# Optimization experiments

Hardware: AMD Instinct MI355X
Metric: run time of the kernel (lower is better)

## Reference

```python
import jax, jax.numpy as jnp
import numpy as np

GN_GROUPS = 32
GN_EPS = 1e-5


def conv3x3(x, w, b=None):
    # x: [B,C,H,W], w: [O,I,3,3]
    y = jax.lax.conv_general_dilated(x, w, (1, 1), 'SAME',
                                     dimension_numbers=('NCHW', 'OIHW', 'NCHW'))
    if b is not None:
        y = y + b[None, :, None, None]
    return y


def group_norm(x, gamma, beta):
    B, C, H, W = x.shape
    xg = x.reshape(B, GN_GROUPS, C // GN_GROUPS, H, W)
    mu = xg.mean(axis=(2, 3, 4), keepdims=True)
    var = ((xg - mu) ** 2).mean(axis=(2, 3, 4), keepdims=True)
    xn = ((xg - mu) * jax.lax.rsqrt(var + GN_EPS)).reshape(B, C, H, W)
    return xn * gamma[None, :, None, None] + beta[None, :, None, None]


def tower(x, ws, gammas, betas):
    # ws: [n_conv, C, C, 3, 3]; conv(bias=False) -> GroupNorm -> ReLU, n_conv times
    for i in range(ws.shape[0]):
        x = jax.nn.relu(group_norm(conv3x3(x, ws[i]), gammas[i], betas[i]))
    return x


def setup_inputs() -> dict:
    key = jax.random.key(0)
    ks = jax.random.split(key, 20)
    C, n_conv, n_fg = 256, 4, 20  # n_class - 1 = 20
    prior = 0.01
    B = 2
    sizes = [(100, 100), (50, 50), (25, 25), (13, 13), (7, 7)]
    inp = {}
    for i, (h, w) in enumerate(sizes):
        inp[f'feat{i}'] = jax.random.normal(ks[i], (B, C, h, w), dtype=jnp.float32)
    std = 0.01  # init_conv_std
    inp['cls_tw_w'] = std * jax.random.normal(ks[5], (n_conv, C, C, 3, 3), dtype=jnp.float32)
    inp['cls_tw_g'] = jnp.ones((n_conv, C), dtype=jnp.float32)
    inp['cls_tw_b'] = jnp.zeros((n_conv, C), dtype=jnp.float32)
    inp['box_tw_w'] = std * jax.random.normal(ks[6], (n_conv, C, C, 3, 3), dtype=jnp.float32)
    inp['box_tw_g'] = jnp.ones((n_conv, C), dtype=jnp.float32)
    inp['box_tw_b'] = jnp.zeros((n_conv, C), dtype=jnp.float32)
    inp['cls_pred_w'] = std * jax.random.normal(ks[7], (n_fg, C, 3, 3), dtype=jnp.float32)
    prior_bias = -np.log((1.0 - prior) / prior)
    inp['cls_pred_b'] = jnp.full((n_fg,), prior_bias, dtype=jnp.float32)
    inp['box_pred_w'] = std * jax.random.normal(ks[8], (4, C, 3, 3), dtype=jnp.float32)
    inp['box_pred_b'] = jnp.zeros((4,), dtype=jnp.float32)
    inp['ctr_pred_w'] = std * jax.random.normal(ks[9], (1, C, 3, 3), dtype=jnp.float32)
    inp['ctr_pred_b'] = jnp.zeros((1,), dtype=jnp.float32)
    inp['scales'] = jnp.ones((5,), dtype=jnp.float32)
    return inp


def reference(feat0, feat1, feat2, feat3, feat4,
              cls_tw_w, cls_tw_g, cls_tw_b,
              box_tw_w, box_tw_g, box_tw_b,
              cls_pred_w, cls_pred_b,
              box_pred_w, box_pred_b,
              ctr_pred_w, ctr_pred_b,
              scales):
    feats = [feat0, feat1, feat2, feat3, feat4]
    logits, bboxes, centers = [], [], []
    for i, feat in enumerate(feats):
        c = tower(feat, cls_tw_w, cls_tw_g, cls_tw_b)
        logits.append(conv3x3(c, cls_pred_w, cls_pred_b))
        centers.append(conv3x3(c, ctr_pred_w, ctr_pred_b))
        b = tower(feat, box_tw_w, box_tw_g, box_tw_b)
        bboxes.append(jnp.exp(conv3x3(b, box_pred_w, box_pred_b) * scales[i]))
    return tuple(logits + bboxes + centers)
```

## Files before the change

### kernel.cpp

```cpp
#include <hip/hip_runtime.h>
#include <hip/hip_bf16.h>
#include <cstdint>

typedef unsigned short u16;
typedef __attribute__((ext_vector_type(8))) short short8;
typedef __attribute__((ext_vector_type(4))) float floatx4;

#define PA_TOTAL 13696
#define CCH 256
#define KTOT 2304

struct Tables {
  int H[5], W[5], P[5], base[5], tile0[5];
  int lb[5], bb[5], cb[5];
};
struct FeatPtrs { const float* f[5]; };
struct ConvArgs {
  const u16* X[2];
  const u16* Wt[2];
  const u16* zbuf;
  u16* outB[2];
  float* stats;
  float* dout;
  const float* biasCls; const float* biasCtr; const float* biasBox; const float* scales;
};

__device__ __forceinline__ u16 f2bf(float f) {
  union { float f; unsigned u; } v; v.f = f;
  unsigned r = v.u + 0x7fffu + ((v.u >> 16) & 1u);
  return (u16)(r >> 16);
}
__device__ __forceinline__ float bf2f(u16 h) {
  union { unsigned u; float f; } v; v.u = ((unsigned)h) << 16;
  return v.f;
}

__device__ __forceinline__ void gl2lds16(const u16* g, u16* l) {
  __builtin_amdgcn_global_load_lds((const __attribute__((address_space(1))) unsigned int*)g,
                                   (__attribute__((address_space(3))) unsigned int*)l, 16, 0, 0);
}

__global__ void reorder_rows(const float* __restrict__ src, u16* __restrict__ out) {
  __shared__ float row[KTOT];
  const int r = blockIdx.x;
  const float* s = src + (size_t)r * KTOT;
  u16* o = out + (size_t)r * KTOT;
#pragma unroll
  for (int j = 0; j < 9; ++j) row[threadIdx.x + j * 256] = s[threadIdx.x + j * 256];
  __syncthreads();
#pragma unroll
  for (int j = 0; j < 9; ++j) {
    int k = threadIdx.x + j * 256;
    o[k] = f2bf(row[(k & 255) * 9 + (k >> 8)]);
  }
}

__global__ void reorder_pred_cls(const float* __restrict__ cls_w, const float* __restrict__ ctr_w,
                                 u16* __restrict__ out) {
  __shared__ float row[KTOT];
  const int r = blockIdx.x;
  const float* s = (r < 20) ? (cls_w + (size_t)r * KTOT) : ctr_w;
  u16* o = out + (size_t)r * KTOT;
#pragma unroll
  for (int j = 0; j < 9; ++j) row[threadIdx.x + j * 256] = s[threadIdx.x + j * 256];
  __syncthreads();
#pragma unroll
  for (int j = 0; j < 9; ++j) {
    int k = threadIdx.x + j * 256;
    o[k] = f2bf(row[(k & 255) * 9 + (k >> 8)]);
  }
}

__global__ void convert_inputs(FeatPtrs fp, u16* __restrict__ out, Tables tb) {
  __shared__ float tile[32][33];
  const int pt = blockIdx.x, c32 = blockIdx.y, b = blockIdx.z;
  const int p0 = pt * 32;
  int lvl = 0;
#pragma unroll
  for (int i = 1; i < 5; ++i) if (p0 >= tb.base[i]) lvl = i;
  const int P = tb.P[lvl];
  const int pl0 = p0 - tb.base[lvl];
  const int r = threadIdx.x >> 5, col = threadIdx.x & 31;
  const float* src = fp.f[lvl] + ((size_t)b * CCH + c32 * 32) * P;
#pragma unroll
  for (int i = 0; i < 4; ++i) {
    int crow = r + i * 8;
    int pl = pl0 + col;
    tile[crow][col] = (pl < P) ? src[(size_t)crow * P + pl] : 0.f;
  }
  __syncthreads();
#pragma unroll
  for (int i = 0; i < 4; ++i) {
    int px = r + i * 8;
    out[((size_t)b * PA_TOTAL + p0 + px) * CCH + c32 * 32 + col] = f2bf(tile[col][px]);
  }
}

template <int MODE>
__global__ __launch_bounds__(256) void conv_mfma(ConvArgs a, Tables tb) {
  constexpr int NI = (MODE == 0) ? 4 : 1;
  const int L = blockIdx.x + (MODE == 0 ? 107 : 108) * (blockIdx.y + 2 * blockIdx.z);
  const int xcd = L & 7, slot = L >> 3;
  int tower, mt, b, t;
  if (MODE == 0) {
    tower = xcd >> 2; mt = (xcd >> 1) & 1; b = xcd & 1; t = slot;
  } else {
    tower = xcd >> 2; mt = 0; b = (xcd >> 1) & 1; t = slot * 2 + (xcd & 1);
    if (t >= 107) return;
  }
  int lvl = 0;
#pragma unroll
  for (int i = 1; i < 5; ++i) if (t >= tb.tile0[i]) lvl = i;
  const int H = tb.H[lvl], W = tb.W[lvl], P = tb.P[lvl], base = tb.base[lvl];
  const int n0 = (t - tb.tile0[lvl]) * 128;

  const int tid = threadIdx.x;
  const int lane = tid & 63, wv = tid >> 6;
  const int wm = wv >> 1, wn = wv & 1;

  __shared__ u16 ldsX[128 * 64];
  __shared__ u16 ldsW[(MODE == 0 ? 128 : 32) * 64];

  const u16* X = a.X[tower];
  const u16* Wt = a.Wt[tower];
  const u16* zbuf = a.zbuf;

  const int qsw = (((lane & 7) ^ (lane >> 3))) * 8;
  int prow[4];
  unsigned mask9[4];
  int ldso[4];
#pragma unroll
  for (int t4 = 0; t4 < 4; ++t4) {
    int row = (t4 * 4 + wv) * 8 + (lane >> 3);
    prow[t4] = n0 + row;
    int rr = prow[t4] / W, cc = prow[t4] - rr * W;
    unsigned m = 0;
#pragma unroll
    for (int tap = 0; tap < 9; ++tap) {
      const int dh = tap / 3 - 1, dw = tap % 3 - 1;
      bool v = ((unsigned)(rr + dh) < (unsigned)H) & ((unsigned)(cc + dw) < (unsigned)W);
      m |= ((unsigned)v) << tap;
    }
    mask9[t4] = m;
    ldso[t4] = (t4 * 4 + wv) * 512;
  }
  const u16* wsrc[4];
#pragma unroll
  for (int t4 = 0; t4 < NI; ++t4) {
    int wrow = (MODE == 0) ? ((t4 * 4 + wv) * 8 + (lane >> 3)) : (wv * 8 + (lane >> 3));
    wsrc[t4] = Wt + (size_t)(mt * 128 + wrow) * KTOT + qsw;
  }
  const u16* Xbp = X + ((size_t)b * PA_TOTAL + base) * CCH;

  const int arow = lane & 15, rsw = lane & 7, kq0 = lane >> 4;
  int aoff[2][4], boff[2][4];
#pragma unroll
  for (int h = 0; h < 2; ++h) {
    int csw = (((h * 4 + kq0) ^ rsw)) * 8;
#pragma unroll
    for (int i = 0; i < NI; ++i) {
      int rowb = (MODE == 0) ? (wm * 64 + i * 16) : (wm * 16);
      aoff[h][i] = (rowb + arow) * 64 + csw;
    }
#pragma unroll
    for (int i = 0; i < 4; ++i) boff[h][i] = (wn * 64 + i * 16 + arow) * 64 + csw;
  }

  floatx4 acc[NI][4];
#pragma unroll
  for (int i = 0; i < NI; ++i)
#pragma unroll
    for (int j = 0; j < 4; ++j) acc[i][j] = (floatx4)0.f;

#pragma unroll 1
  for (int icb = 0; icb < 4; ++icb) {
#pragma unroll
    for (int tap = 0; tap < 9; ++tap) {
      const int dh = tap / 3 - 1, dw = tap % 3 - 1;
      const int dpos = dh * W + dw;
      const int ko = tap * 256 + icb * 64;
      __syncthreads();
#pragma unroll
      for (int t4 = 0; t4 < 4; ++t4) {
        const u16* src = ((mask9[t4] >> tap) & 1)
            ? (Xbp + (size_t)(prow[t4] + dpos) * CCH + qsw + icb * 64) : zbuf;
        gl2lds16(src, ldsX + ldso[t4]);
      }
#pragma unroll
      for (int t4 = 0; t4 < NI; ++t4)
        gl2lds16(wsrc[t4] + ko, ldsW + (MODE == 0 ? ldso[t4] : wv * 512));
      __syncthreads();
#pragma unroll
      for (int h = 0; h < 2; ++h) {
        short8 af[NI], bv[4];
#pragma unroll
        for (int i = 0; i < NI; ++i) af[i] = *(const short8*)(ldsW + aoff[h][i]);
#pragma unroll
        for (int j = 0; j < 4; ++j) bv[j] = *(const short8*)(ldsX + boff[h][j]);
#pragma unroll
        for (int i = 0; i < NI; ++i)
#pragma unroll
          for (int j = 0; j < 4; ++j)
            acc[i][j] = __builtin_amdgcn_mfma_f32_16x16x32_bf16(af[i], bv[j], acc[i][j], 0, 0, 0);
      }
    }
  }

  const int quad = lane >> 4, col = lane & 15;
  if (MODE == 0) {
    u16* convB = a.outB[tower];
    float s[4] = {0.f, 0.f, 0.f, 0.f}, ss[4] = {0.f, 0.f, 0.f, 0.f};
#pragma unroll
    for (int j = 0; j < 4; ++j) {
      int pl = n0 + wn * 64 + j * 16 + col;
      bool valid = pl < P;
      u16* dst = convB + ((size_t)b * PA_TOTAL + base + pl) * CCH + mt * 128 + wm * 64 + quad * 4;
#pragma unroll
      for (int i = 0; i < 4; ++i) {
        ushort4 hv;
#pragma unroll
        for (int r = 0; r < 4; ++r) {
          u16 hh = f2bf(acc[i][j][r]);
          ((u16*)&hv)[r] = hh;
          float vr = bf2f(hh);
          if (valid) { s[i] += vr; ss[i] += vr * vr; }
        }
        if (valid) *(ushort4*)(dst + i * 16) = hv;
      }
    }
#pragma unroll
    for (int i = 0; i < 4; ++i) {
#pragma unroll
      for (int off = 16; off >= 1; off >>= 1) {
        s[i] += __shfl_down(s[i], off, 64);
        ss[i] += __shfl_down(ss[i], off, 64);
      }
    }
    if ((lane & 31) == 0) {
      int half = lane >> 5;
#pragma unroll
      for (int i = 0; i < 4; ++i) {
        float* st = a.stats + tower * 640 +
                    ((size_t)((b * 5 + lvl) * 32 + mt * 16 + wm * 8 + i * 2 + half)) * 2;
        atomicAdd(st, s[i]);
        atomicAdd(st + 1, ss[i]);
      }
    }
  } else {
    float* dout = a.dout;
    if (tower == 0) {
#pragma unroll
      for (int j = 0; j < 4; ++j) {
        int pl = n0 + wn * 64 + j * 16 + col;
        if (pl >= P) continue;
        int ocb = wm * 16 + quad * 4;
#pragma unroll
        for (int r = 0; r < 4; ++r) {
          int oc = ocb + r;
          float v = acc[0][j][r];
          if (oc < 20)       dout[tb.lb[lvl] + ((size_t)b * 20 + oc) * P + pl] = v + a.biasCls[oc];
          else if (oc == 20) dout[tb.cb[lvl] + (size_t)b * P + pl] = v + a.biasCtr[0];
        }
      }
    } else {
      float sc = a.scales[lvl];
#pragma unroll
      for (int j = 0; j < 4; ++j) {
        int pl = n0 + wn * 64 + j * 16 + col;
        if (pl >= P) continue;
        int ocb = wm * 16 + quad * 4;
#pragma unroll
        for (int r = 0; r < 4; ++r) {
          int oc = ocb + r;
          if (oc < 4)
            dout[tb.bb[lvl] + ((size_t)b * 4 + oc) * P + pl] = expf((acc[0][j][r] + a.biasBox[oc]) * sc);
        }
      }
    }
  }
}

__global__ void gn_norm(const u16* __restrict__ c0, const u16* __restrict__ c1,
                        const float* __restrict__ stats,
                        const float* __restrict__ g0, const float* __restrict__ b0,
                        const float* __restrict__ g1, const float* __restrict__ b1,
                        u16* __restrict__ a0, u16* __restrict__ a1, Tables tb) {
  const int tower = blockIdx.y;
  const u16* convB = tower ? c1 : c0;
  const float* gamma = tower ? g1 : g0;
  const float* beta = tower ? b1 : b0;
  u16* act = tower ? a1 : a0;
  int idx = blockIdx.x * 256 + threadIdx.x;
  int c8 = idx & 31;
  int rest = idx >> 5;
  int p = rest % PA_TOTAL;
  int b = rest / PA_TOTAL;
  int lvl = 0;
#pragma unroll
  for (int i = 1; i < 5; ++i) if (p >= tb.base[i]) lvl = i;
  if (p - tb.base[lvl] >= tb.P[lvl]) return;
  const float* st = stats + tower * 640 + ((size_t)((b * 5 + lvl) * 32 + c8)) * 2;
  float cnt = 8.f * (float)tb.P[lvl];
  float mean = st[0] / cnt;
  float var = st[1] / cnt - mean * mean;
  float inv = rsqrtf(var + 1e-5f);
  const short8 x = *(const short8*)(convB + ((size_t)b * PA_TOTAL + p) * CCH + c8 * 8);
  short8 o;
#pragma unroll
  for (int j = 0; j < 8; ++j) {
    float v = bf2f((u16)x[j]);
    float y = (v - mean) * inv * gamma[c8 * 8 + j] + beta[c8 * 8 + j];
    y = fmaxf(y, 0.f);
    o[j] = (short)f2bf(y);
  }
  *(short8*)(act + ((size_t)b * PA_TOTAL + p) * CCH + c8 * 8) = o;
}

extern "C" void kernel_launch(void* const* d_in, const int* in_sizes, int n_in,
                              void* d_out, int out_size, void* d_ws, size_t ws_size,
                              hipStream_t stream) {
  const float* feat[5];
  for (int i = 0; i < 5; ++i) feat[i] = (const float*)d_in[i];
  const float* cls_tw_w  = (const float*)d_in[5];
  const float* cls_tw_g  = (const float*)d_in[6];
  const float* cls_tw_b  = (const float*)d_in[7];
  const float* box_tw_w  = (const float*)d_in[8];
  const float* box_tw_g  = (const float*)d_in[9];
  const float* box_tw_b  = (const float*)d_in[10];
  const float* cls_pred_w = (const float*)d_in[11];
  const float* cls_pred_b = (const float*)d_in[12];
  const float* box_pred_w = (const float*)d_in[13];
  const float* box_pred_b = (const float*)d_in[14];
  const float* ctr_pred_w = (const float*)d_in[15];
  const float* ctr_pred_b = (const float*)d_in[16];
  const float* scales     = (const float*)d_in[17];
  float* out = (float*)d_out;

  char* ws = (char*)d_ws;
  u16*   zbuf   = (u16*)(ws);
  float* stats  = (float*)(ws + 512);
  u16*   WrCls  = (u16*)(ws + 8192);
  u16*   WrBox  = (u16*)(ws + 8192 + 4718592);
  u16*   WrPCls = (u16*)(ws + 8192 + 2 * 4718592);
  u16*   WrPBox = (u16*)(ws + 8192 + 2 * 4718592 + 589824);
  u16*   bufIn   = (u16*)(ws + 10625024);
  u16*   bufAct0 = (u16*)(ws + 10625024 + 1 * (size_t)14024704);
  u16*   bufAct1 = (u16*)(ws + 10625024 + 2 * (size_t)14024704);
  u16*   bufCv0  = (u16*)(ws + 10625024 + 3 * (size_t)14024704);
  u16*   bufCv1  = (u16*)(ws + 10625024 + 4 * (size_t)14024704);

  Tables tb = { {100,50,25,13,7}, {100,50,25,13,7}, {10000,2500,625,169,49},
                {0,10112,12672,13312,13568}, {0,79,99,104,106},
                {0,400000,500000,525000,531760},
                {533720,613720,633720,638720,640072},
                {640464,660464,665464,666714,667052} };

  hipMemsetAsync(zbuf, 0, 512, stream);
  hipMemsetAsync(WrPCls, 0, 589824, stream);
  hipMemsetAsync(WrPBox, 0, 589824, stream);

  reorder_rows<<<1024, 256, 0, stream>>>(cls_tw_w, WrCls);
  reorder_rows<<<1024, 256, 0, stream>>>(box_tw_w, WrBox);
  reorder_pred_cls<<<21, 256, 0, stream>>>(cls_pred_w, ctr_pred_w, WrPCls);
  reorder_rows<<<4, 256, 0, stream>>>(box_pred_w, WrPBox);

  FeatPtrs fp = {{feat[0], feat[1], feat[2], feat[3], feat[4]}};
  convert_inputs<<<dim3(PA_TOTAL / 32, 8, 2), 256, 0, stream>>>(fp, bufIn, tb);

  ConvArgs a;
  a.zbuf = zbuf; a.stats = stats; a.dout = out;
  a.biasCls = cls_pred_b; a.biasCtr = ctr_pred_b; a.biasBox = box_pred_b; a.scales = scales;
  a.outB[0] = bufCv0; a.outB[1] = bufCv1;

  for (int s = 0; s < 4; ++s) {
    a.X[0] = (s == 0) ? bufIn : bufAct0;
    a.X[1] = (s == 0) ? bufIn : bufAct1;
    a.Wt[0] = WrCls + (size_t)s * 256 * KTOT;
    a.Wt[1] = WrBox + (size_t)s * 256 * KTOT;
    hipMemsetAsync(stats, 0, 5120, stream);
    conv_mfma<0><<<dim3(107, 2, 4), 256, 0, stream>>>(a, tb);
    gn_norm<<<dim3(3424, 2), 256, 0, stream>>>(bufCv0, bufCv1, stats,
                                               cls_tw_g + s * 256, cls_tw_b + s * 256,
                                               box_tw_g + s * 256, box_tw_b + s * 256,
                                               bufAct0, bufAct1, tb);
  }
  a.X[0] = bufAct0; a.X[1] = bufAct1;
  a.Wt[0] = WrPCls; a.Wt[1] = WrPBox;
  conv_mfma<1><<<dim3(108, 2, 2), 256, 0, stream>>>(a, tb);
}
```

Before: 645.3 us.

## Share weight tile across two pixel tiles in 512-thread tower conv blocks

The tower conv kernel now runs 512-thread blocks where two 4-wave groups each compute a different 128-pixel tile but share one 128x64 weight tile in LDS. Each wave loads only half as many weight rows, which halves weight global traffic and LDS weight fill per output tile. The grid halves to 54 blocks per dimension, with a padding tile masked out when the tile count is odd. The prediction conv is split into its own non-templated kernel with unchanged behaviour. The larger blocks use more LDS and registers per block, which may lower occupancy or scheduling flexibility.

```diff
diff --git a/kernel.cpp b/kernel.cpp
--- a/kernel.cpp
+++ b/kernel.cpp
@@ -96,18 +96,161 @@
   }
 }
 
-template <int MODE>
-__global__ __launch_bounds__(256) void conv_mfma(ConvArgs a, Tables tb) {
-  constexpr int NI = (MODE == 0) ? 4 : 1;
-  const int L = blockIdx.x + (MODE == 0 ? 107 : 108) * (blockIdx.y + 2 * blockIdx.z);
+__global__ __launch_bounds__(512) void conv_tower(ConvArgs a, Tables tb) {
+  const int L = blockIdx.x + 54 * (blockIdx.y + 2 * blockIdx.z);
   const int xcd = L & 7, slot = L >> 3;
-  int tower, mt, b, t;
-  if (MODE == 0) {
-    tower = xcd >> 2; mt = (xcd >> 1) & 1; b = xcd & 1; t = slot;
-  } else {
-    tower = xcd >> 2; mt = 0; b = (xcd >> 1) & 1; t = slot * 2 + (xcd & 1);
-    if (t >= 107) return;
-  }
+  const int tower = xcd >> 2, mt = (xcd >> 1) & 1, b = xcd & 1;
+
+  const int tid = threadIdx.x;
+  const int lane = tid & 63, wv = tid >> 6;
+  const int g = wv >> 2, wg = wv & 3;
+  const int wm = wg >> 1, wn = wg & 1;
+
+  const int t = 2 * slot + g;
+  const bool tvalid = (t < 107);
+  const int te = tvalid ? t : 106;
+  int lvl = 0;
+#pragma unroll
+  for (int i = 1; i < 5; ++i) if (te >= tb.tile0[i]) lvl = i;
+  const int H = tb.H[lvl], W = tb.W[lvl], P = tb.P[lvl], base = tb.base[lvl];
+  const int n0 = (te - tb.tile0[lvl]) * 128;
+
+  __shared__ u16 ldsX[2 * 128 * 64];
+  __shared__ u16 ldsW[128 * 64];
+
+  const u16* X = a.X[tower];
+  const u16* Wt = a.Wt[tower];
+  const u16* zbuf = a.zbuf;
+
+  const int qsw = (((lane & 7) ^ (lane >> 3))) * 8;
+  int prow[4];
+  unsigned mask9[4];
+  int ldso[4];
+#pragma unroll
+  for (int t4 = 0; t4 < 4; ++t4) {
+    int row = (t4 * 4 + wg) * 8 + (lane >> 3);
+    prow[t4] = n0 + row;
+    int rr = prow[t4] / W, cc = prow[t4] - rr * W;
+    unsigned m = 0;
+    if (tvalid) {
+#pragma unroll
+      for (int tap = 0; tap < 9; ++tap) {
+        const int dh = tap / 3 - 1, dw = tap % 3 - 1;
+        bool v = ((unsigned)(rr + dh) < (unsigned)H) & ((unsigned)(cc + dw) < (unsigned)W);
+        m |= ((unsigned)v) << tap;
+      }
+    }
+    mask9[t4] = m;
+    ldso[t4] = g * 8192 + (t4 * 4 + wg) * 512;
+  }
+  const u16* wsrc[2];
+#pragma unroll
+  for (int e = 0; e < 2; ++e) {
+    int wrow = wv * 16 + e * 8 + (lane >> 3);
+    wsrc[e] = Wt + (size_t)(mt * 128 + wrow) * KTOT + qsw;
+  }
+  const u16* Xbp = X + ((size_t)b * PA_TOTAL + base) * CCH;
+
+  const int arow = lane & 15, rsw = lane & 7, kq0 = lane >> 4;
+  int aoff[2][4], boff[2][4];
+#pragma unroll
+  for (int h = 0; h < 2; ++h) {
+    int csw = (((h * 4 + kq0) ^ rsw)) * 8;
+#pragma unroll
+    for (int i = 0; i < 4; ++i) {
+      aoff[h][i] = (wm * 64 + i * 16 + arow) * 64 + csw;
+      boff[h][i] = g * 8192 + (wn * 64 + i * 16 + arow) * 64 + csw;
+    }
+  }
+
+  floatx4 acc[4][4];
+#pragma unroll
+  for (int i = 0; i < 4; ++i)
+#pragma unroll
+    for (int j = 0; j < 4; ++j) acc[i][j] = (floatx4)0.f;
+
+#pragma unroll 1
+  for (int icb = 0; icb < 4; ++icb) {
+#pragma unroll
+    for (int tap = 0; tap < 9; ++tap) {
+      const int dh = tap / 3 - 1, dw = tap % 3 - 1;
+      const int dpos = dh * W + dw;
+      const int ko = tap * 256 + icb * 64;
+      __syncthreads();
+#pragma unroll
+      for (int t4 = 0; t4 < 4; ++t4) {
+        const u16* src = ((mask9[t4] >> tap) & 1)
+            ? (Xbp + (size_t)(prow[t4] + dpos) * CCH + qsw + icb * 64) : zbuf;
+        gl2lds16(src, ldsX + ldso[t4]);
+      }
+#pragma unroll
+      for (int e = 0; e < 2; ++e)
+        gl2lds16(wsrc[e] + ko, ldsW + wv * 1024 + e * 512);
+      __syncthreads();
+#pragma unroll
+      for (int h = 0; h < 2; ++h) {
+        short8 af[4], bv[4];
+#pragma unroll
+        for (int i = 0; i < 4; ++i) af[i] = *(const short8*)(ldsW + aoff[h][i]);
+#pragma unroll
+        for (int j = 0; j < 4; ++j) bv[j] = *(const short8*)(ldsX + boff[h][j]);
+#pragma unroll
+        for (int i = 0; i < 4; ++i)
+#pragma unroll
+          for (int j = 0; j < 4; ++j)
+            acc[i][j] = __builtin_amdgcn_mfma_f32_16x16x32_bf16(af[i], bv[j], acc[i][j], 0, 0, 0);
+      }
+    }
+  }
+
+  if (!tvalid) return;
+  const int quad = lane >> 4, col = lane & 15;
+  u16* convB = a.outB[tower];
+  float s[4] = {0.f, 0.f, 0.f, 0.f}, ss[4] = {0.f, 0.f, 0.f, 0.f};
+#pragma unroll
+  for (int j = 0; j < 4; ++j) {
+    int pl = n0 + wn * 64 + j * 16 + col;
+    bool valid = pl < P;
+    u16* dst = convB + ((size_t)b * PA_TOTAL + base + pl) * CCH + mt * 128 + wm * 64 + quad * 4;
+#pragma unroll
+    for (int i = 0; i < 4; ++i) {
+      ushort4 hv;
+#pragma unroll
+      for (int r = 0; r < 4; ++r) {
+        u16 hh = f2bf(acc[i][j][r]);
+        ((u16*)&hv)[r] = hh;
+        float vr = bf2f(hh);
+        if (valid) { s[i] += vr; ss[i] += vr * vr; }
+      }
+      if (valid) *(ushort4*)(dst + i * 16) = hv;
+    }
+  }
+#pragma unroll
+  for (int i = 0; i < 4; ++i) {
+#pragma unroll
+    for (int off = 16; off >= 1; off >>= 1) {
+      s[i] += __shfl_down(s[i], off, 64);
+      ss[i] += __shfl_down(ss[i], off, 64);
+    }
+  }
+  if ((lane & 31) == 0) {
+    int half = lane >> 5;
+#pragma unroll
+    for (int i = 0; i < 4; ++i) {
+      float* st = a.stats + tower * 640 +
+                  ((size_t)((b * 5 + lvl) * 32 + mt * 16 + wm * 8 + i * 2 + half)) * 2;
+      atomicAdd(st, s[i]);
+      atomicAdd(st + 1, ss[i]);
+    }
+  }
+}
+
+__global__ __launch_bounds__(256) void conv_pred(ConvArgs a, Tables tb) {
+  const int L = blockIdx.x + 108 * (blockIdx.y + 2 * blockIdx.z);
+  const int xcd = L & 7, slot = L >> 3;
+  const int tower = xcd >> 2, b = (xcd >> 1) & 1;
+  const int t = slot * 2 + (xcd & 1);
+  if (t >= 107) return;
   int lvl = 0;
 #pragma unroll
   for (int i = 1; i < 5; ++i) if (t >= tb.tile0[i]) lvl = i;
@@ -119,7 +262,7 @@
   const int wm = wv >> 1, wn = wv & 1;
 
   __shared__ u16 ldsX[128 * 64];
-  __shared__ u16 ldsW[(MODE == 0 ? 128 : 32) * 64];
+  __shared__ u16 ldsW[32 * 64];
 
   const u16* X = a.X[tower];
   const u16* Wt = a.Wt[tower];
@@ -144,33 +287,22 @@
     mask9[t4] = m;
     ldso[t4] = (t4 * 4 + wv) * 512;
   }
-  const u16* wsrc[4];
-#pragma unroll
-  for (int t4 = 0; t4 < NI; ++t4) {
-    int wrow = (MODE == 0) ? ((t4 * 4 + wv) * 8 + (lane >> 3)) : (wv * 8 + (lane >> 3));
-    wsrc[t4] = Wt + (size_t)(mt * 128 + wrow) * KTOT + qsw;
-  }
+  const u16* wsrc = Wt + (size_t)(wv * 8 + (lane >> 3)) * KTOT + qsw;
   const u16* Xbp = X + ((size_t)b * PA_TOTAL + base) * CCH;
 
   const int arow = lane & 15, rsw = lane & 7, kq0 = lane >> 4;
-  int aoff[2][4], boff[2][4];
+  int aoff[2], boff[2][4];
 #pragma unroll
   for (int h = 0; h < 2; ++h) {
     int csw = (((h * 4 + kq0) ^ rsw)) * 8;
-#pragma unroll
-    for (int i = 0; i < NI; ++i) {
-      int rowb = (MODE == 0) ? (wm * 64 + i * 16) : (wm * 16);
-      aoff[h][i] = (rowb + arow) * 64 + csw;
-    }
+    aoff[h] = (wm * 16 + arow) * 64 + csw;
 #pragma unroll
     for (int i = 0; i < 4; ++i) boff[h][i] = (wn * 64 + i * 16 + arow) * 64 + csw;
   }
 
-  floatx4 acc[NI][4];
-#pragma unroll
-  for (int i = 0; i < NI; ++i)
-#pragma unroll
-    for (int j = 0; j < 4; ++j) acc[i][j] = (floatx4)0.f;
+  floatx4 acc[4];
+#pragma unroll
+  for (int j = 0; j < 4; ++j) acc[j] = (floatx4)0.f;
 
 #pragma unroll 1
   for (int icb = 0; icb < 4; ++icb) {
@@ -186,95 +318,48 @@
             ? (Xbp + (size_t)(prow[t4] + dpos) * CCH + qsw + icb * 64) : zbuf;
         gl2lds16(src, ldsX + ldso[t4]);
       }
-#pragma unroll
-      for (int t4 = 0; t4 < NI; ++t4)
-        gl2lds16(wsrc[t4] + ko, ldsW + (MODE == 0 ? ldso[t4] : wv * 512));
+      gl2lds16(wsrc + ko, ldsW + wv * 512);
       __syncthreads();
 #pragma unroll
       for (int h = 0; h < 2; ++h) {
-        short8 af[NI], bv[4];
-#pragma unroll
-        for (int i = 0; i < NI; ++i) af[i] = *(const short8*)(ldsW + aoff[h][i]);
-#pragma unroll
-        for (int j = 0; j < 4; ++j) bv[j] = *(const short8*)(ldsX + boff[h][j]);
-#pragma unroll
-        for (int i = 0; i < NI; ++i)
-#pragma unroll
-          for (int j = 0; j < 4; ++j)
-            acc[i][j] = __builtin_amdgcn_mfma_f32_16x16x32_bf16(af[i], bv[j], acc[i][j], 0, 0, 0);
+        short8 af = *(const short8*)(ldsW + aoff[h]);
+#pragma unroll
+        for (int j = 0; j < 4; ++j) {
+          short8 bv = *(const short8*)(ldsX + boff[h][j]);
+          acc[j] = __builtin_amdgcn_mfma_f32_16x16x32_bf16(af, bv, acc[j], 0, 0, 0);
+        }
       }
     }
   }
 
   const int quad = lane >> 4, col = lane & 15;
-  if (MODE == 0) {
-    u16* convB = a.outB[tower];
-    float s[4] = {0.f, 0.f, 0.f, 0.f}, ss[4] = {0.f, 0.f, 0.f, 0.f};
+  float* dout = a.dout;
+  if (tower == 0) {
 #pragma unroll
     for (int j = 0; j < 4; ++j) {
       int pl = n0 + wn * 64 + j * 16 + col;
-      bool valid = pl < P;
-      u16* dst = convB + ((size_t)b * PA_TOTAL + base + pl) * CCH + mt * 128 + wm * 64 + quad * 4;
-#pragma unroll
-      for (int i = 0; i < 4; ++i) {
-        ushort4 hv;
-#pragma unroll
-        for (int r = 0; r < 4; ++r) {
-          u16 hh = f2bf(acc[i][j][r]);
-          ((u16*)&hv)[r] = hh;
-          float vr = bf2f(hh);
-          if (valid) { s[i] += vr; ss[i] += vr * vr; }
-        }
-        if (valid) *(ushort4*)(dst + i * 16) = hv;
-      }
-    }
-#pragma unroll
-    for (int i = 0; i < 4; ++i) {
-#pragma unroll
-      for (int off = 16; off >= 1; off >>= 1) {
-        s[i] += __shfl_down(s[i], off, 64);
-        ss[i] += __shfl_down(ss[i], off, 64);
-      }
-    }
-    if ((lane & 31) == 0) {
-      int half = lane >> 5;
-#pragma unroll
-      for (int i = 0; i < 4; ++i) {
-        float* st = a.stats + tower * 640 +
-                    ((size_t)((b * 5 + lvl) * 32 + mt * 16 + wm * 8 + i * 2 + half)) * 2;
-        atomicAdd(st, s[i]);
-        atomicAdd(st + 1, ss[i]);
+      if (pl >= P) continue;
+      int ocb = wm * 16 + quad * 4;
+#pragma unroll
+      for (int r = 0; r < 4; ++r) {
+        int oc = ocb + r;
+        float v = acc[j][r];
+        if (oc < 20)       dout[tb.lb[lvl] + ((size_t)b * 20 + oc) * P + pl] = v + a.biasCls[oc];
+        else if (oc == 20) dout[tb.cb[lvl] + (size_t)b * P + pl] = v + a.biasCtr[0];
       }
     }
   } else {
-    float* dout = a.dout;
-    if (tower == 0) {
-#pragma unroll
-      for (int j = 0; j < 4; ++j) {
-        int pl = n0 + wn * 64 + j * 16 + col;
-        if (pl >= P) continue;
-        int ocb = wm * 16 + quad * 4;
-#pragma unroll
-        for (int r = 0; r < 4; ++r) {
-          int oc = ocb + r;
-          float v = acc[0][j][r];
-          if (oc < 20)       dout[tb.lb[lvl] + ((size_t)b * 20 + oc) * P + pl] = v + a.biasCls[oc];
-          else if (oc == 20) dout[tb.cb[lvl] + (size_t)b * P + pl] = v + a.biasCtr[0];
-        }
-      }
-    } else {
-      float sc = a.scales[lvl];
-#pragma unroll
-      for (int j = 0; j < 4; ++j) {
-        int pl = n0 + wn * 64 + j * 16 + col;
-        if (pl >= P) continue;
-        int ocb = wm * 16 + quad * 4;
-#pragma unroll
-        for (int r = 0; r < 4; ++r) {
-          int oc = ocb + r;
-          if (oc < 4)
-            dout[tb.bb[lvl] + ((size_t)b * 4 + oc) * P + pl] = expf((acc[0][j][r] + a.biasBox[oc]) * sc);
-        }
+    float sc = a.scales[lvl];
+#pragma unroll
+    for (int j = 0; j < 4; ++j) {
+      int pl = n0 + wn * 64 + j * 16 + col;
+      if (pl >= P) continue;
+      int ocb = wm * 16 + quad * 4;
+#pragma unroll
+      for (int r = 0; r < 4; ++r) {
+        int oc = ocb + r;
+        if (oc < 4)
+          dout[tb.bb[lvl] + ((size_t)b * 4 + oc) * P + pl] = expf((acc[j][r] + a.biasBox[oc]) * sc);
       }
     }
   }
@@ -378,7 +463,7 @@
     a.Wt[0] = WrCls + (size_t)s * 256 * KTOT;
     a.Wt[1] = WrBox + (size_t)s * 256 * KTOT;
     hipMemsetAsync(stats, 0, 5120, stream);
-    conv_mfma<0><<<dim3(107, 2, 4), 256, 0, stream>>>(a, tb);
+    conv_tower<<<dim3(54, 2, 4), 512, 0, stream>>>(a, tb);
     gn_norm<<<dim3(3424, 2), 256, 0, stream>>>(bufCv0, bufCv1, stats,
                                                cls_tw_g + s * 256, cls_tw_b + s * 256,
                                                box_tw_g + s * 256, box_tw_b + s * 256,
@@ -386,5 +471,5 @@
   }
   a.X[0] = bufAct0; a.X[1] = bufAct1;
   a.Wt[0] = WrPCls; a.Wt[1] = WrPBox;
-  conv_mfma<1><<<dim3(108, 2, 2), 256, 0, stream>>>(a, tb);
-}
+  conv_pred<<<dim3(108, 2, 2), 256, 0, stream>>>(a, tb);
+}
```

Result: slower. 722.9 us (+12.0%).

## Prefetch next tap tiles into registers instead of direct global-to-LDS loads

Applied to the files above, without the earlier changes.

Replaces the global_load_lds direct copies with register staging. Each step writes the previously loaded X and weight vectors into LDS, then issues global loads for the next tap/channel block into registers. The MFMAs of the current step run while those loads are in flight. This is software pipelining that hides global latency behind compute, at the cost of extra VGPRs and explicit LDS store instructions. It also drops the zero buffer in favour of a zero register.

```diff
diff --git a/kernel.cpp b/kernel.cpp
--- a/kernel.cpp
+++ b/kernel.cpp
@@ -5,6 +5,7 @@
 typedef unsigned short u16;
 typedef __attribute__((ext_vector_type(8))) short short8;
 typedef __attribute__((ext_vector_type(4))) float floatx4;
+typedef __attribute__((ext_vector_type(4))) int intx4;
 
 #define PA_TOTAL 13696
 #define CCH 256
@@ -35,11 +36,6 @@
   return v.f;
 }
 
-__device__ __forceinline__ void gl2lds16(const u16* g, u16* l) {
-  __builtin_amdgcn_global_load_lds((const __attribute__((address_space(1))) unsigned int*)g,
-                                   (__attribute__((address_space(3))) unsigned int*)l, 16, 0, 0);
-}
-
 __global__ void reorder_rows(const float* __restrict__ src, u16* __restrict__ out) {
   __shared__ float row[KTOT];
   const int r = blockIdx.x;
@@ -123,12 +119,11 @@
 
   const u16* X = a.X[tower];
   const u16* Wt = a.Wt[tower];
-  const u16* zbuf = a.zbuf;
 
   const int qsw = (((lane & 7) ^ (lane >> 3))) * 8;
   int prow[4];
   unsigned mask9[4];
-  int ldso[4];
+  int xdst[4];
 #pragma unroll
   for (int t4 = 0; t4 < 4; ++t4) {
     int row = (t4 * 4 + wv) * 8 + (lane >> 3);
@@ -142,18 +137,20 @@
       m |= ((unsigned)v) << tap;
     }
     mask9[t4] = m;
-    ldso[t4] = (t4 * 4 + wv) * 512;
-  }
-  const u16* wsrc[4];
-#pragma unroll
-  for (int t4 = 0; t4 < NI; ++t4) {
-    int wrow = (MODE == 0) ? ((t4 * 4 + wv) * 8 + (lane >> 3)) : (wv * 8 + (lane >> 3));
-    wsrc[t4] = Wt + (size_t)(mt * 128 + wrow) * KTOT + qsw;
+    xdst[t4] = (t4 * 4 + wv) * 1024 + lane * 16;
+  }
+  const u16* wsrc[NI];
+  int wdst[NI];
+#pragma unroll
+  for (int e = 0; e < NI; ++e) {
+    int wrow = (MODE == 0) ? ((e * 4 + wv) * 8 + (lane >> 3)) : (wv * 8 + (lane >> 3));
+    wsrc[e] = Wt + (size_t)(mt * 128 + wrow) * KTOT + qsw;
+    wdst[e] = (MODE == 0) ? xdst[e] : (wv * 1024 + lane * 16);
   }
   const u16* Xbp = X + ((size_t)b * PA_TOTAL + base) * CCH;
 
   const int arow = lane & 15, rsw = lane & 7, kq0 = lane >> 4;
-  int aoff[2][4], boff[2][4];
+  int aoff[2][NI], boff[2][4];
 #pragma unroll
   for (int h = 0; h < 2; ++h) {
     int csw = (((h * 4 + kq0) ^ rsw)) * 8;
@@ -172,23 +169,40 @@
 #pragma unroll
     for (int j = 0; j < 4; ++j) acc[i][j] = (floatx4)0.f;
 
+  const intx4 zreg = {0, 0, 0, 0};
+  intx4 xr[4], wr[NI];
+  {
+    const int dpos0 = -W - 1;
+#pragma unroll
+    for (int t4 = 0; t4 < 4; ++t4)
+      xr[t4] = (mask9[t4] & 1)
+          ? *(const intx4*)(Xbp + (size_t)(prow[t4] + dpos0) * CCH + qsw) : zreg;
+#pragma unroll
+    for (int e = 0; e < NI; ++e) wr[e] = *(const intx4*)(wsrc[e]);
+  }
+
 #pragma unroll 1
   for (int icb = 0; icb < 4; ++icb) {
 #pragma unroll
     for (int tap = 0; tap < 9; ++tap) {
-      const int dh = tap / 3 - 1, dw = tap % 3 - 1;
-      const int dpos = dh * W + dw;
-      const int ko = tap * 256 + icb * 64;
       __syncthreads();
 #pragma unroll
-      for (int t4 = 0; t4 < 4; ++t4) {
-        const u16* src = ((mask9[t4] >> tap) & 1)
-            ? (Xbp + (size_t)(prow[t4] + dpos) * CCH + qsw + icb * 64) : zbuf;
-        gl2lds16(src, ldsX + ldso[t4]);
-      }
-#pragma unroll
-      for (int t4 = 0; t4 < NI; ++t4)
-        gl2lds16(wsrc[t4] + ko, ldsW + (MODE == 0 ? ldso[t4] : wv * 512));
+      for (int t4 = 0; t4 < 4; ++t4) *(intx4*)((char*)ldsX + xdst[t4]) = xr[t4];
+#pragma unroll
+      for (int e = 0; e < NI; ++e) *(intx4*)((char*)ldsW + wdst[e]) = wr[e];
+      if (!(icb == 3 && tap == 8)) {
+        const int ntap = (tap == 8) ? 0 : tap + 1;
+        const int nicb = (tap == 8) ? icb + 1 : icb;
+        const int ndh = ntap / 3;
+        const int ndpos = (ndh - 1) * W + (ntap - 3 * ndh - 1);
+        const int nko = ntap * 256 + nicb * 64;
+#pragma unroll
+        for (int t4 = 0; t4 < 4; ++t4)
+          xr[t4] = ((mask9[t4] >> ntap) & 1)
+              ? *(const intx4*)(Xbp + (size_t)(prow[t4] + ndpos) * CCH + qsw + nicb * 64) : zreg;
+#pragma unroll
+        for (int e = 0; e < NI; ++e) wr[e] = *(const intx4*)(wsrc[e] + nko);
+      }
       __syncthreads();
 #pragma unroll
       for (int h = 0; h < 2; ++h) {
```

Result: no change. 642.0 us (-0.5%).
